# Performance work log

Hardware: AMD Instinct MI355X
Metric: run time of the kernel (lower is better)

The kernel has to match this reference:

```python
import jax, jax.numpy as jnp
import numpy as np

# Paired binary-tree layout over 20 inputs: widths 20->10->5->3->2->1.
# Odd trailing element is carried through unchanged. Node counts per layer
# sum to 19 nodes per tree; 19 trees total.
LAYER_WIDTHS = [20, 10, 5, 3, 2]  # widths at the input of each pairing layer
NODE_COUNTS = [10, 5, 2, 1, 1]    # pairs formed at each layer (sum = 19)
EPS = 1e-6


def setup_inputs() -> dict:
    key = jax.random.key(0)
    k1, k2, k3, k4 = jax.random.split(key, 4)
    B = 1_000_000
    p1 = jax.random.randint(k1, (B,), 0, 10)
    p2 = jax.random.randint(k2, (B,), 0, 10)
    c20 = jax.random.uniform(k3, (B, 20), dtype=jnp.float32)  # fuzzy truth values in [0,1]
    # raw andness params: one per node (19) per tree (19)
    w_raw = jax.random.normal(k4, (19, 19), dtype=jnp.float32)
    return {"p1": p1, "p2": p2, "c20": c20, "w_raw": w_raw}


def _multi_tree_forward(c20, w_raw):
    B = c20.shape[0]
    T = 19  # number of trees
    # andness in (0,1): convex mix between AND (min) and OR (max)
    w = jax.nn.sigmoid(w_raw)  # [T, 19]
    # all 19 trees see the same 20D input -> vectorize trees as a dim
    x = jnp.broadcast_to(c20[:, None, :], (B, T, 20))  # [B, T, 20]
    off = 0
    for width, n in zip(LAYER_WIDTHS, NODE_COUNTS):
        a = x[:, :, 0:2 * n:2]   # left children  [B, T, n]
        b = x[:, :, 1:2 * n:2]   # right children [B, T, n]
        wn = w[:, off:off + n][None, :, :]  # [1, T, n]
        y = wn * jnp.minimum(a, b) + (1.0 - wn) * jnp.maximum(a, b)
        if width % 2 == 1:  # carry the unpaired trailing element through
            y = jnp.concatenate([y, x[:, :, -1:]], axis=-1)
        x = y
        off += n
    out = x[:, :, 0]  # [B, 19] root of each tree
    return jnp.clip(out, EPS, 1.0 - EPS)


def reference(p1, p2, c20, w_raw):
    # p1/p2 are part of the original signature but unused by the forward math
    return _multi_tree_forward(c20, w_raw)
```

## Files before the change

### kernel.cpp

```cpp
#include <hip/hip_runtime.h>

#define EPS_F 1e-6f
#define BLK   256

typedef float v2f __attribute__((ext_vector_type(2)));
typedef float v4f __attribute__((ext_vector_type(4)));

__global__ void sigmoid_w_kernel(const float* __restrict__ w_raw,
                                 float* __restrict__ w) {
    int i = threadIdx.x;
    if (i < 361) {
        w[i] = 1.0f / (1.0f + expf(-w_raw[i]));
    }
}

__device__ __forceinline__ v2f vsplat(float s) {
    v2f r; r.x = s; r.y = s; return r;
}

__device__ __forceinline__ v2f vmix(v2f a, v2f b, float wv) {
    v2f mn, mx;
    mn.x = fminf(a.x, b.x); mn.y = fminf(a.y, b.y);
    mx.x = fmaxf(a.x, b.x); mx.y = fmaxf(a.y, b.y);
    return vsplat(wv) * (mn - mx) + mx;
}

__device__ __forceinline__ float clampf(float r) {
    return __builtin_amdgcn_fmed3f(r, EPS_F, 1.0f - EPS_F);
}

__global__ __launch_bounds__(BLK) void tree_forward_kernel(
    const float* __restrict__ c20,
    const float* __restrict__ w,
    float* __restrict__ out,
    int B)
{
    __shared__ float so[BLK * 19];

    const int tid = threadIdx.x;
    const int S0  = blockIdx.x * (2 * BLK);
    const int sA  = S0 + tid;
    const int sB  = S0 + BLK + tid;

    v2f d[10], mx[10];
    {
        const float4* pA = reinterpret_cast<const float4*>(c20 + (size_t)sA * 20);
        const float4* pB = reinterpret_cast<const float4*>(c20 + (size_t)sB * 20);
        const bool vA = (sA < B), vB = (sB < B);
        #pragma unroll
        for (int q = 0; q < 5; ++q) {
            float4 a4 = vA ? pA[q] : make_float4(0.f, 0.f, 0.f, 0.f);
            float4 b4 = vB ? pB[q] : make_float4(0.f, 0.f, 0.f, 0.f);
            {
                v2f a, b;
                a.x = a4.x; a.y = b4.x;
                b.x = a4.y; b.y = b4.y;
                v2f mn;
                mn.x       = fminf(a.x, b.x); mn.y       = fminf(a.y, b.y);
                mx[2*q].x  = fmaxf(a.x, b.x); mx[2*q].y  = fmaxf(a.y, b.y);
                d[2*q] = mn - mx[2*q];
            }
            {
                v2f a, b;
                a.x = a4.z; a.y = b4.z;
                b.x = a4.w; b.y = b4.w;
                v2f mn;
                mn.x        = fminf(a.x, b.x); mn.y        = fminf(a.y, b.y);
                mx[2*q+1].x = fmaxf(a.x, b.x); mx[2*q+1].y = fmaxf(a.y, b.y);
                d[2*q+1] = mn - mx[2*q+1];
            }
        }
    }

    float oB[19];
    float* __restrict__ o = &so[tid * 19];

    #pragma unroll
    for (int t = 0; t < 19; ++t) {
        const float* wr = w + t * 19;
        v2f z[5];
        #pragma unroll
        for (int k = 0; k < 5; ++k) {
            v2f ya = vsplat(wr[2*k    ]) * d[2*k    ] + mx[2*k    ];
            v2f yb = vsplat(wr[2*k + 1]) * d[2*k + 1] + mx[2*k + 1];
            z[k] = vmix(ya, yb, wr[10 + k]);
        }
        v2f u0 = vmix(z[0], z[1], wr[15]);
        v2f u1 = vmix(z[2], z[3], wr[16]);
        v2f v  = vmix(u0, u1, wr[17]);
        v2f r  = vmix(v, z[4], wr[18]);
        o[t]  = clampf(r.x);
        oB[t] = clampf(r.y);
    }

    __syncthreads();

    const int nDw = B * 19;
    const v4f* ls = reinterpret_cast<const v4f*>(so);

    {
        const int baseDw = S0 * 19;
        #pragma unroll
        for (int i = tid; i < (BLK * 19) / 4; i += BLK) {
            int g = baseDw + i * 4;
            if (g + 3 < nDw) {
                __builtin_nontemporal_store(ls[i], reinterpret_cast<v4f*>(out + g));
            } else if (g < nDw) {
                v4f v4 = ls[i];
                out[g] = v4.x;
                if (g + 1 < nDw) out[g + 1] = v4.y;
                if (g + 2 < nDw) out[g + 2] = v4.z;
            }
        }
    }

    __syncthreads();

    #pragma unroll
    for (int t = 0; t < 19; ++t) o[t] = oB[t];

    __syncthreads();

    {
        const int baseDw = (S0 + BLK) * 19;
        #pragma unroll
        for (int i = tid; i < (BLK * 19) / 4; i += BLK) {
            int g = baseDw + i * 4;
            if (g + 3 < nDw) {
                __builtin_nontemporal_store(ls[i], reinterpret_cast<v4f*>(out + g));
            } else if (g < nDw) {
                v4f v4 = ls[i];
                out[g] = v4.x;
                if (g + 1 < nDw) out[g + 1] = v4.y;
                if (g + 2 < nDw) out[g + 2] = v4.z;
            }
        }
    }
}

extern "C" void kernel_launch(void* const* d_in, const int* in_sizes, int n_in,
                              void* d_out, int out_size, void* d_ws, size_t ws_size,
                              hipStream_t stream) {
    const float* c20   = (const float*)d_in[2];
    const float* w_raw = (const float*)d_in[3];
    float* out = (float*)d_out;
    float* w   = (float*)d_ws;

    int B = in_sizes[0];

    sigmoid_w_kernel<<<1, 384, 0, stream>>>(w_raw, w);

    int grid = (B + 2 * BLK - 1) / (2 * BLK);
    tree_forward_kernel<<<grid, BLK, 0, stream>>>(c20, w, out, B);
}
```

Measured before the change: 159.8 us.

## Vectorize across tree pairs with transposed weights, one sample per thread

The sigmoid kernel now writes the weights transposed (node-major, stride 20), so each thread can load weights for two adjacent trees as one v2f. The packed-math pairing moves from two samples per thread to two trees per thread, with a scalar tail for the 19th tree. Each thread now handles one sample, so the grid doubles and the two-phase shared-memory write-out with its extra barriers goes away. The trade-off is more blocks, less work per thread, and an odd scalar tree that does not use packed math.

```diff
diff --git a/kernel.cpp b/kernel.cpp
--- a/kernel.cpp
+++ b/kernel.cpp
@@ -7,10 +7,12 @@
 typedef float v4f __attribute__((ext_vector_type(4)));
 
 __global__ void sigmoid_w_kernel(const float* __restrict__ w_raw,
-                                 float* __restrict__ w) {
+                                 float* __restrict__ wt) {
     int i = threadIdx.x;
     if (i < 361) {
-        w[i] = 1.0f / (1.0f + expf(-w_raw[i]));
+        int t = i / 19;
+        int k = i % 19;
+        wt[k * 20 + t] = 1.0f / (1.0f + expf(-w_raw[i]));
     }
 }
 
@@ -18,11 +20,11 @@
     v2f r; r.x = s; r.y = s; return r;
 }
 
-__device__ __forceinline__ v2f vmix(v2f a, v2f b, float wv) {
+__device__ __forceinline__ v2f pairmix(v2f a, v2f b, v2f wv) {
     v2f mn, mx;
     mn.x = fminf(a.x, b.x); mn.y = fminf(a.y, b.y);
     mx.x = fmaxf(a.x, b.x); mx.y = fmaxf(a.y, b.y);
-    return vsplat(wv) * (mn - mx) + mx;
+    return wv * (mn - mx) + mx;
 }
 
 __device__ __forceinline__ float clampf(float r) {
@@ -31,109 +33,106 @@
 
 __global__ __launch_bounds__(BLK) void tree_forward_kernel(
     const float* __restrict__ c20,
-    const float* __restrict__ w,
+    const float* __restrict__ wt,
     float* __restrict__ out,
     int B)
 {
     __shared__ float so[BLK * 19];
 
     const int tid = threadIdx.x;
-    const int S0  = blockIdx.x * (2 * BLK);
-    const int sA  = S0 + tid;
-    const int sB  = S0 + BLK + tid;
+    const int S0  = blockIdx.x * BLK;
+    const int s   = S0 + tid;
 
-    v2f d[10], mx[10];
+    float mx[10], d[10];
     {
-        const float4* pA = reinterpret_cast<const float4*>(c20 + (size_t)sA * 20);
-        const float4* pB = reinterpret_cast<const float4*>(c20 + (size_t)sB * 20);
-        const bool vA = (sA < B), vB = (sB < B);
+        const float4* p = reinterpret_cast<const float4*>(c20 + (size_t)s * 20);
+        const bool valid = (s < B);
         #pragma unroll
         for (int q = 0; q < 5; ++q) {
-            float4 a4 = vA ? pA[q] : make_float4(0.f, 0.f, 0.f, 0.f);
-            float4 b4 = vB ? pB[q] : make_float4(0.f, 0.f, 0.f, 0.f);
+            float4 v = valid ? p[q] : make_float4(0.f, 0.f, 0.f, 0.f);
             {
-                v2f a, b;
-                a.x = a4.x; a.y = b4.x;
-                b.x = a4.y; b.y = b4.y;
-                v2f mn;
-                mn.x       = fminf(a.x, b.x); mn.y       = fminf(a.y, b.y);
-                mx[2*q].x  = fmaxf(a.x, b.x); mx[2*q].y  = fmaxf(a.y, b.y);
-                d[2*q] = mn - mx[2*q];
+                float mn = fminf(v.x, v.y);
+                mx[2*q] = fmaxf(v.x, v.y);
+                d[2*q]  = mn - mx[2*q];
             }
             {
-                v2f a, b;
-                a.x = a4.z; a.y = b4.z;
-                b.x = a4.w; b.y = b4.w;
-                v2f mn;
-                mn.x        = fminf(a.x, b.x); mn.y        = fminf(a.y, b.y);
-                mx[2*q+1].x = fmaxf(a.x, b.x); mx[2*q+1].y = fmaxf(a.y, b.y);
-                d[2*q+1] = mn - mx[2*q+1];
+                float mn = fminf(v.z, v.w);
+                mx[2*q+1] = fmaxf(v.z, v.w);
+                d[2*q+1]  = mn - mx[2*q+1];
             }
         }
     }
 
-    float oB[19];
     float* __restrict__ o = &so[tid * 19];
 
     #pragma unroll
-    for (int t = 0; t < 19; ++t) {
-        const float* wr = w + t * 19;
+    for (int tp = 0; tp < 9; ++tp) {
+        const float* wp = wt + 2 * tp;
+
+        v2f y[10];
+        #pragma unroll
+        for (int k = 0; k < 10; ++k) {
+            v2f wk = *reinterpret_cast<const v2f*>(wp + 20 * k);
+            y[k] = wk * vsplat(d[k]) + vsplat(mx[k]);
+        }
+
         v2f z[5];
         #pragma unroll
         for (int k = 0; k < 5; ++k) {
-            v2f ya = vsplat(wr[2*k    ]) * d[2*k    ] + mx[2*k    ];
-            v2f yb = vsplat(wr[2*k + 1]) * d[2*k + 1] + mx[2*k + 1];
-            z[k] = vmix(ya, yb, wr[10 + k]);
+            v2f wk = *reinterpret_cast<const v2f*>(wp + 20 * (10 + k));
+            z[k] = pairmix(y[2*k], y[2*k+1], wk);
         }
-        v2f u0 = vmix(z[0], z[1], wr[15]);
-        v2f u1 = vmix(z[2], z[3], wr[16]);
-        v2f v  = vmix(u0, u1, wr[17]);
-        v2f r  = vmix(v, z[4], wr[18]);
-        o[t]  = clampf(r.x);
-        oB[t] = clampf(r.y);
+
+        v2f u0 = pairmix(z[0], z[1], *reinterpret_cast<const v2f*>(wp + 20 * 15));
+        v2f u1 = pairmix(z[2], z[3], *reinterpret_cast<const v2f*>(wp + 20 * 16));
+        v2f v  = pairmix(u0, u1,   *reinterpret_cast<const v2f*>(wp + 20 * 17));
+        v2f r  = pairmix(v, z[4],  *reinterpret_cast<const v2f*>(wp + 20 * 18));
+
+        o[2*tp]     = clampf(r.x);
+        o[2*tp + 1] = clampf(r.y);
+    }
+
+    {
+        const float* wr = wt + 18;
+        float y[10];
+        #pragma unroll
+        for (int k = 0; k < 10; ++k)
+            y[k] = fmaf(wr[20 * k], d[k], mx[k]);
+        float z[5];
+        #pragma unroll
+        for (int k = 0; k < 5; ++k) {
+            float mn = fminf(y[2*k], y[2*k+1]);
+            float mxx = fmaxf(y[2*k], y[2*k+1]);
+            z[k] = fmaf(wr[20 * (10 + k)], mn - mxx, mxx);
+        }
+        float mn, mxx;
+        mn = fminf(z[0], z[1]); mxx = fmaxf(z[0], z[1]);
+        float u0 = fmaf(wr[20 * 15], mn - mxx, mxx);
+        mn = fminf(z[2], z[3]); mxx = fmaxf(z[2], z[3]);
+        float u1 = fmaf(wr[20 * 16], mn - mxx, mxx);
+        mn = fminf(u0, u1); mxx = fmaxf(u0, u1);
+        float v0 = fmaf(wr[20 * 17], mn - mxx, mxx);
+        mn = fminf(v0, z[4]); mxx = fmaxf(v0, z[4]);
+        float rr = fmaf(wr[20 * 18], mn - mxx, mxx);
+        o[18] = clampf(rr);
     }
 
     __syncthreads();
 
-    const int nDw = B * 19;
+    const int nDw    = B * 19;
+    const int baseDw = S0 * 19;
     const v4f* ls = reinterpret_cast<const v4f*>(so);
 
-    {
-        const int baseDw = S0 * 19;
-        #pragma unroll
-        for (int i = tid; i < (BLK * 19) / 4; i += BLK) {
-            int g = baseDw + i * 4;
-            if (g + 3 < nDw) {
-                __builtin_nontemporal_store(ls[i], reinterpret_cast<v4f*>(out + g));
-            } else if (g < nDw) {
-                v4f v4 = ls[i];
-                out[g] = v4.x;
-                if (g + 1 < nDw) out[g + 1] = v4.y;
-                if (g + 2 < nDw) out[g + 2] = v4.z;
-            }
-        }
-    }
-
-    __syncthreads();
-
     #pragma unroll
-    for (int t = 0; t < 19; ++t) o[t] = oB[t];
-
-    __syncthreads();
-
-    {
-        const int baseDw = (S0 + BLK) * 19;
-        #pragma unroll
-        for (int i = tid; i < (BLK * 19) / 4; i += BLK) {
-            int g = baseDw + i * 4;
-            if (g + 3 < nDw) {
-                __builtin_nontemporal_store(ls[i], reinterpret_cast<v4f*>(out + g));
-            } else if (g < nDw) {
-                v4f v4 = ls[i];
-                out[g] = v4.x;
-                if (g + 1 < nDw) out[g + 1] = v4.y;
-                if (g + 2 < nDw) out[g + 2] = v4.z;
-            }
+    for (int i = tid; i < (BLK * 19) / 4; i += BLK) {
+        int g = baseDw + i * 4;
+        if (g + 3 < nDw) {
+            __builtin_nontemporal_store(ls[i], reinterpret_cast<v4f*>(out + g));
+        } else if (g < nDw) {
+            v4f v4 = ls[i];
+            out[g] = v4.x;
+            if (g + 1 < nDw) out[g + 1] = v4.y;
+            if (g + 2 < nDw) out[g + 2] = v4.z;
         }
     }
 }
@@ -144,12 +143,12 @@
     const float* c20   = (const float*)d_in[2];
     const float* w_raw = (const float*)d_in[3];
     float* out = (float*)d_out;
-    float* w   = (float*)d_ws;
+    float* wt  = (float*)d_ws;
 
     int B = in_sizes[0];
 
-    sigmoid_w_kernel<<<1, 384, 0, stream>>>(w_raw, w);
+    sigmoid_w_kernel<<<1, 384, 0, stream>>>(w_raw, wt);
 
-    int grid = (B + 2 * BLK - 1) / (2 * BLK);
-    tree_forward_kernel<<<grid, BLK, 0, stream>>>(c20, w, out, B);
+    int grid = (B + BLK - 1) / BLK;
+    tree_forward_kernel<<<grid, BLK, 0, stream>>>(c20, wt, out, B);
 }
```

After: 153.8 us. 1.04x faster.
